# Kernel optimization log

Measured on AMD Instinct MI355X. Metric: run time of the kernel, lower is better.

Reference implementation:

```python
import jax, jax.numpy as jnp
import numpy as np

N, E, A, S = 100000, 1600000, 500000, 50000
F_IN, W, LAYERS = 64, 64, 3


def setup_inputs() -> dict:
    key = jax.random.key(0)
    ks = jax.random.split(key, 20)

    def glorot(k, shape):
        fan_in = shape[-2]
        return jax.random.normal(k, shape, dtype=jnp.float32) / jnp.sqrt(jnp.float32(fan_in))

    return {
        "x": jax.random.normal(ks[0], (N, F_IN), dtype=jnp.float32),
        "edge_src": jax.random.randint(ks[1], (E,), 0, N, dtype=jnp.int32),
        "edge_dst": jax.random.randint(ks[2], (E,), 0, N, dtype=jnp.int32),
        "gather_idx": jax.random.randint(ks[3], (A,), 0, N, dtype=jnp.int32),
        "seg_idx": jax.random.randint(ks[4], (A,), 0, S, dtype=jnp.int32),
        # GraphConv 0: lin_root (no bias) + lin_rel (bias)
        "w_root0": glorot(ks[5], (F_IN, W)),
        "w_rel0": glorot(ks[6], (F_IN, W)),
        "b0": jnp.zeros((W,), jnp.float32),
        # hidden GraphConv layers, stacked
        "w_root_h": glorot(ks[7], (LAYERS - 1, W, W)),
        "w_rel_h": glorot(ks[8], (LAYERS - 1, W, W)),
        "b_h": jnp.zeros((LAYERS - 1, W), jnp.float32),
        # MLP head
        "fc1_w": glorot(ks[9], (W, W)),
        "fc1_b": jnp.zeros((W,), jnp.float32),
        "fc2_w": glorot(ks[10], (W, 32)),
        "fc2_b": jnp.zeros((32,), jnp.float32),
        "fc3_w": glorot(ks[11], (32, 2)),
        "fc3_b": jnp.zeros((2,), jnp.float32),
        "num_sets": S,
    }


def _graph_conv(h, edge_src, edge_dst, w_root, w_rel, b):
    # PyG GraphConv (aggr='add'): out_i = W_root h_i + W_rel * sum_{j->i} h_j + b
    agg = jax.ops.segment_sum(h[edge_src], edge_dst, num_segments=h.shape[0])
    return h @ w_root + agg @ w_rel + b


def reference(x, edge_src, edge_dst, gather_idx, seg_idx,
              w_root0, w_rel0, b0, w_root_h, w_rel_h, b_h,
              fc1_w, fc1_b, fc2_w, fc2_b, fc3_w, fc3_b, num_sets):
    h = jax.nn.elu(_graph_conv(x, edge_src, edge_dst, w_root0, w_rel0, b0))
    for i in range(w_root_h.shape[0]):
        h = jax.nn.elu(_graph_conv(h, edge_src, edge_dst, w_root_h[i], w_rel_h[i], b_h[i]))
    # set pooling: gather node rows then scatter_add into sets
    pooled = jax.ops.segment_sum(h[gather_idx], seg_idx, num_segments=num_sets)  # [S, W]
    h = jax.nn.elu(pooled @ fc1_w + fc1_b)
    # dropout p=0.5 is identity at inference
    h = jax.nn.elu(h @ fc2_w + fc2_b)
    logits = h @ fc3_w + fc3_b
    return jax.nn.log_softmax(logits, axis=1)
```

## Files before the change

kernel.cpp:

```cpp
#include <hip/hip_runtime.h>


#define FEAT 64
#define SH 9
#define BSZ 512
#define CH 512
#define CAP 12288
#define SCHUNK 1024
#define IDXE 256
#define HPAD 8
#define LCHUNK 3200

typedef unsigned short u16;
typedef unsigned char u8;
typedef __attribute__((ext_vector_type(8))) short bf16x8;
typedef __attribute__((ext_vector_type(4))) float f32x4;
typedef __attribute__((ext_vector_type(2))) float f32x2;

__device__ __forceinline__ float bf2f(u16 u) {
  union { unsigned int i; float f; } c; c.i = ((unsigned int)u) << 16; return c.f;
}
__device__ __forceinline__ u16 f2bf(float f) {
  union { float f; unsigned int i; } c; c.f = f;
  unsigned int u = c.i;
  return (u16)((u + 0x7FFFu + ((u >> 16) & 1u)) >> 16);
}

__device__ __forceinline__ unsigned pack_fp8x4(float a, float b, float c, float d) {
  int lo = __builtin_amdgcn_cvt_pk_fp8_f32(a, b, 0, 0);
  return (unsigned)__builtin_amdgcn_cvt_pk_fp8_f32(c, d, lo, 1);
}
__device__ __forceinline__ float4 unpack_fp8x4(unsigned v) {
  f32x2 lo = __builtin_amdgcn_cvt_pk_f32_fp8(v, 0);
  f32x2 hi = __builtin_amdgcn_cvt_pk_f32_fp8(v, 1);
  float4 r; r.x = lo.x; r.y = lo.y; r.z = hi.x; r.w = hi.y;
  return r;
}

__global__ void p1a2f_kernel(const int* __restrict__ kE, int* __restrict__ cE, int nE, int NBe,
                             const int* __restrict__ kP, int* __restrict__ cP, int nP, int NBp,
                             const float* __restrict__ x, u16* __restrict__ xb,
                             u8* __restrict__ xb8, int n4, int g_cvt,
                             const float* __restrict__ wr0, const float* __restrict__ wl0,
                             const float* __restrict__ wrh, const float* __restrict__ wlh,
                             u16* __restrict__ wpack) {
  __shared__ int hist[256];
  int tid = threadIdx.x, b = blockIdx.x;
  if (b < 2 * CH) {
    const int* keys; int* counts; int nK, NB, c;
    if (b < CH) { keys = kE; counts = cE; nK = nE; NB = NBe; c = b; }
    else        { keys = kP; counts = cP; nK = nP; NB = NBp; c = b - CH; }
    hist[tid] = 0;
    __syncthreads();
    int len = (nK + CH - 1) / CH;
    int cbeg = c * len, cend = min(nK, cbeg + len);
    for (int i = cbeg + tid; i < cend; i += 256) atomicAdd(&hist[keys[i] >> SH], 1);
    __syncthreads();
    if (tid < NB) counts[tid * CH + c] = hist[tid];
  } else if (b < 2 * CH + g_cvt) {
    int i = (b - 2 * CH) * 256 + tid;
    if (i < n4) {
      float4 v = ((const float4*)x)[i];
      ushort4 o = { f2bf(v.x), f2bf(v.y), f2bf(v.z), f2bf(v.w) };
      ((ushort4*)xb)[i] = o;
      ((unsigned*)xb8)[i] = pack_fp8x4(v.x, v.y, v.z, v.w);
    }
  } else {
    int t4 = (b - 2 * CH - g_cvt) * 4 + (tid >> 6);
    if (t4 < 48) {
      int l = t4 >> 4, t = t4 & 15;
      int kt = t >> 2, nt = t & 3;
      int lane = tid & 63;
      const float* wr; const float* wl;
      if (l == 0) { wr = wr0; wl = wl0; }
      else        { wr = wrh + (l - 1) * FEAT * FEAT; wl = wlh + (l - 1) * FEAT * FEAT; }
      int n = nt * 16 + (lane & 15);
      int k0 = kt * 32 + (lane >> 4) * 8;
      u16* dst = wpack + (((size_t)l * 16 + t) * 64 + lane) * 8;
#pragma unroll
      for (int j = 0; j < 8; ++j) {
        int k = k0 + j;
        float v = (k < FEAT) ? wr[k * FEAT + n] : wl[(k - FEAT) * FEAT + n];
        dst[j] = f2bf(v);
      }
    } else if (t4 == 48) {
      int lane = tid & 63;
      int Nn = n4 >> 4;
      if (lane < 16) {
        ushort4 z = {0, 0, 0, 0};
        ((ushort4*)(xb + (size_t)Nn * FEAT))[lane] = z;
      } else if (lane < 32) {
        ((unsigned*)(xb8 + (size_t)Nn * FEAT))[lane & 15] = 0u;
      }
    }
  }
}

__global__ void scan1_kernel(int* __restrict__ d0, int* __restrict__ bs0, int L0, int nb0,
                             int* __restrict__ d1, int* __restrict__ bs1, int L1) {
  __shared__ int tsum[256];
  int tid = threadIdx.x, b = blockIdx.x;
  int* data; int* bsums; int L, c;
  if (b < nb0) { data = d0; bsums = bs0; L = L0; c = b; }
  else         { data = d1; bsums = bs1; L = L1; c = b - nb0; }
  int base = c * SCHUNK + tid * 4;
  int v[4];
#pragma unroll
  for (int i = 0; i < 4; ++i) v[i] = (base + i < L) ? data[base + i] : 0;
  int local = v[0] + v[1] + v[2] + v[3];
  tsum[tid] = local;
  __syncthreads();
  for (int off = 1; off < 256; off <<= 1) {
    int u = (tid >= off) ? tsum[tid - off] : 0;
    __syncthreads();
    tsum[tid] += u;
    __syncthreads();
  }
  int excl = tsum[tid] - local;
  if (tid == 255) bsums[c] = tsum[255];
  int run = excl;
#pragma unroll
  for (int i = 0; i < 4; ++i) {
    if (base + i < L) data[base + i] = run;
    run += v[i];
  }
}

__global__ void scan3_kernel(int* __restrict__ d0, const int* __restrict__ bs0,
                             int* __restrict__ bb0, int L0, int NB0, int tot0, int nb0, int g0,
                             int* __restrict__ d1, const int* __restrict__ bs1,
                             int* __restrict__ bb1, int L1, int NB1, int tot1, int nb1) {
  __shared__ int t[256];
  int b = blockIdx.x, tid = threadIdx.x;
  int* data; const int* bsums; int* bbase; int L, NB, tot, nb, i;
  if (b < g0) { data = d0; bsums = bs0; bbase = bb0; L = L0; NB = NB0; tot = tot0; nb = nb0; i = b * 256 + tid; }
  else        { data = d1; bsums = bs1; bbase = bb1; L = L1; NB = NB1; tot = tot1; nb = nb1; i = (b - g0) * 256 + tid; }
  int v = (tid < nb) ? bsums[tid] : 0;
  t[tid] = v;
  __syncthreads();
  for (int off = 1; off < 256; off <<= 1) {
    int u = (tid >= off) ? t[tid - off] : 0;
    __syncthreads();
    t[tid] += u;
    __syncthreads();
  }
  int incl = t[tid];
  __syncthreads();
  t[tid] = incl - v;
  __syncthreads();
  if (i < L) {
    int val = data[i] + t[i / SCHUNK];
    data[i] = val;
    if ((i & (CH - 1)) == 0) bbase[i / CH] = val;
  }
  if (i == 0) bbase[NB] = tot;
}

__global__ void __launch_bounds__(256)
p1b2_kernel(const int* __restrict__ s0, const int* __restrict__ k0,
            const int* __restrict__ c0, int* __restrict__ bin0, int n0, int NB0,
            const int* __restrict__ s1, const int* __restrict__ k1,
            const int* __restrict__ c1, int* __restrict__ bin1, int n1, int NB1) {
  __shared__ int s_bin[LCHUNK];
  __shared__ unsigned char s_bu[LCHUNK];
  __shared__ int lcur[256];
  __shared__ int gdiff[256];
  __shared__ int ts[256];
  int tid = threadIdx.x, b = blockIdx.x;
  const int* src; const int* keys; const int* counts; int* bin; int nE, NB, c;
  if (b < CH) { src = s0; keys = k0; counts = c0; bin = bin0; nE = n0; NB = NB0; c = b; }
  else        { src = s1; keys = k1; counts = c1; bin = bin1; nE = n1; NB = NB1; c = b - CH; }
  int len = (nE + CH - 1) / CH;
  int cbeg = c * len, cend = min(nE, cbeg + len);
  int L = cend - cbeg;

  int cur = 0, v = 0;
  if (tid < NB) {
    int f = tid * CH + c;
    cur = counts[f];
    int nxt = (f + 1 < NB * CH) ? counts[f + 1] : nE;
    v = nxt - cur;
  }
  ts[tid] = v;
  __syncthreads();
  for (int off = 1; off < 256; off <<= 1) {
    int u = (tid >= off) ? ts[tid - off] : 0;
    __syncthreads();
    ts[tid] += u;
    __syncthreads();
  }
  int excl = ts[tid] - v;
  lcur[tid] = excl;
  gdiff[tid] = cur - excl;
  __syncthreads();

  if (L <= LCHUNK) {
    for (int i = cbeg + tid; i < cend; i += 256) {
      int k = keys[i];
      int bu = k >> SH;
      int pos = atomicAdd(&lcur[bu], 1);
      s_bin[pos] = (src[i] << SH) | (k & (BSZ - 1));
      s_bu[pos] = (unsigned char)bu;
    }
    __syncthreads();
    for (int i = tid; i < L; i += 256) {
      int bu = s_bu[i];
      bin[gdiff[bu] + i] = s_bin[i];
    }
  } else {
    for (int i = cbeg + tid; i < cend; i += 256) {
      int k = keys[i];
      int bu = k >> SH;
      int pos = atomicAdd(&lcur[bu], 1);
      bin[gdiff[bu] + pos] = (src[i] << SH) | (k & (BSZ - 1));
    }
  }
}

__global__ void __launch_bounds__(256) p2_kernel(const int* __restrict__ bin0,
                                                 const int* __restrict__ bb0,
                                                 int* __restrict__ csr0, int* __restrict__ rs0,
                                                 int nn0, int NB0,
                                                 const int* __restrict__ bin1,
                                                 const int* __restrict__ bb1,
                                                 int* __restrict__ csr1, int* __restrict__ rs1,
                                                 int nn1) {
  __shared__ int s_csr[CAP];
  __shared__ int hist[BSZ];
  __shared__ int excl[BSZ];
  __shared__ int ts[256];
  int tid = threadIdx.x, bb = blockIdx.x;
  const int* bin; const int* bbase; int* csr; int* rs; int n_nodes, b;
  if (bb < NB0) { bin = bin0; bbase = bb0; csr = csr0; rs = rs0; n_nodes = nn0; b = bb; }
  else          { bin = bin1; bbase = bb1; csr = csr1; rs = rs1; n_nodes = nn1; b = bb - NB0; }
  int base = bbase[b];
  int cnt = bbase[b + 1] - base;
  int node_lo = b * BSZ;
  int nnode = min(BSZ, n_nodes - node_lo);

  hist[tid] = 0; hist[tid + 256] = 0;
  __syncthreads();
  for (int i = tid; i < cnt; i += 256) atomicAdd(&hist[bin[base + i] & (BSZ - 1)], 1);
  __syncthreads();

  int a0 = hist[2 * tid], a1 = hist[2 * tid + 1];
  int pair = a0 + a1;
  ts[tid] = pair;
  __syncthreads();
  for (int off = 1; off < 256; off <<= 1) {
    int u = (tid >= off) ? ts[tid - off] : 0;
    __syncthreads();
    ts[tid] += u;
    __syncthreads();
  }
  int pexcl = ts[tid] - pair;
  excl[2 * tid] = pexcl;
  excl[2 * tid + 1] = pexcl + a0;
  __syncthreads();

  for (int t = tid; t < nnode; t += 256) rs[node_lo + t] = base + excl[t];
  if (tid == 0 && node_lo + nnode >= n_nodes) rs[n_nodes] = bbase[(n_nodes + BSZ - 1) / BSZ];
  hist[tid] = excl[tid]; hist[tid + 256] = excl[tid + 256];
  __syncthreads();

  if (cnt <= CAP) {
    for (int i = tid; i < cnt; i += 256) {
      int e = bin[base + i];
      int pos = atomicAdd(&hist[e & (BSZ - 1)], 1);
      s_csr[pos] = e >> SH;
    }
    __syncthreads();
    for (int i = tid; i < cnt; i += 256) csr[base + i] = s_csr[i];
  } else {
    for (int i = tid; i < cnt; i += 256) {
      int e = bin[base + i];
      int pos = atomicAdd(&hist[e & (BSZ - 1)], 1);
      csr[base + pos] = e >> SH;
    }
  }
}

__device__ __forceinline__ float4 reduce_sub(float4 a) {
  a.x += __shfl_xor(a.x, 16, 64); a.y += __shfl_xor(a.y, 16, 64);
  a.z += __shfl_xor(a.z, 16, 64); a.w += __shfl_xor(a.w, 16, 64);
  a.x += __shfl_xor(a.x, 32, 64); a.y += __shfl_xor(a.y, 32, 64);
  a.z += __shfl_xor(a.z, 32, 64); a.w += __shfl_xor(a.w, 32, 64);
  return a;
}

struct RowB { ushort4 a, b, c, e; };

__device__ __forceinline__ RowB load_b16(const u16* __restrict__ hb, const int* idx,
                                         int i, int d, int ch, int sent) {
  int j0 = idx[i], j1 = idx[i + 4], j2 = idx[i + 8], j3 = idx[i + 12];
  j0 = (i      < d) ? j0 : sent;
  j1 = (i + 4  < d) ? j1 : sent;
  j2 = (i + 8  < d) ? j2 : sent;
  j3 = (i + 12 < d) ? j3 : sent;
  RowB r;
  r.a = ((const ushort4*)(hb + (size_t)((unsigned)(j0 * FEAT))))[ch];
  r.b = ((const ushort4*)(hb + (size_t)((unsigned)(j1 * FEAT))))[ch];
  r.c = ((const ushort4*)(hb + (size_t)((unsigned)(j2 * FEAT))))[ch];
  r.e = ((const ushort4*)(hb + (size_t)((unsigned)(j3 * FEAT))))[ch];
  return r;
}

__device__ __forceinline__ float4 acc_b16(float4 acc, RowB r) {
  acc.x += (bf2f(r.a.x) + bf2f(r.b.x)) + (bf2f(r.c.x) + bf2f(r.e.x));
  acc.y += (bf2f(r.a.y) + bf2f(r.b.y)) + (bf2f(r.c.y) + bf2f(r.e.y));
  acc.z += (bf2f(r.a.z) + bf2f(r.b.z)) + (bf2f(r.c.z) + bf2f(r.e.z));
  acc.w += (bf2f(r.a.w) + bf2f(r.b.w)) + (bf2f(r.c.w) + bf2f(r.e.w));
  return acc;
}

template <class FW>
__device__ __forceinline__ void gather8(const u16* __restrict__ hb,
                                        const int* __restrict__ rs,
                                        const int* __restrict__ csr,
                                        int* sidx, int wbase, int n, int sent,
                                        int sub, int ch, int lane, FW&& wr) {
  int r[9];
#pragma unroll
  for (int j = 0; j < 9; ++j) r[j] = rs[min(wbase + j, n)];
  int rbeg = r[0];
  int run = r[8] - rbeg;
  const int* eb;
  if (run <= IDXE) {
    for (int i = lane; i < run; i += 64) sidx[i] = csr[rbeg + i];
    eb = sidx;
  } else {
    eb = csr + rbeg;
  }
  int nt = min(8, n - wbase);
  if (nt == 8) {
    RowB fn = load_b16(hb, eb, sub, r[1] - r[0], ch, sent);
#pragma unroll
    for (int t = 0; t < 8; ++t) {
      int off = r[t] - rbeg;
      int d = r[t + 1] - r[t];
      RowB cur = fn;
      if (t < 7) fn = load_b16(hb, eb + (r[t + 1] - rbeg), sub, r[t + 2] - r[t + 1], ch, sent);
      float4 acc = {0.f, 0.f, 0.f, 0.f};
      for (int i = sub + 16; i < d; i += 16) {
        RowB nx = load_b16(hb, eb + off, i, d, ch, sent);
        acc = acc_b16(acc, cur);
        cur = nx;
      }
      acc = acc_b16(acc, cur);
      wr(t, reduce_sub(acc));
    }
  } else {
    for (int t = 0; t < nt; ++t) {
      int off = r[t] - rbeg;
      int d = r[t + 1] - r[t];
      float4 acc = {0.f, 0.f, 0.f, 0.f};
      for (int i = sub; i < d; i += 16)
        acc = acc_b16(acc, load_b16(hb, eb + off, i, d, ch, sent));
      wr(t, reduce_sub(acc));
    }
  }
}

struct Row8 { unsigned a, b, c, e; };

__device__ __forceinline__ Row8 load_b8(const u8* __restrict__ h8, const int* idx,
                                        int i, int d, int ch, int sent) {
  int j0 = idx[i], j1 = idx[i + 4], j2 = idx[i + 8], j3 = idx[i + 12];
  j0 = (i      < d) ? j0 : sent;
  j1 = (i + 4  < d) ? j1 : sent;
  j2 = (i + 8  < d) ? j2 : sent;
  j3 = (i + 12 < d) ? j3 : sent;
  Row8 r;
  r.a = ((const unsigned*)(h8 + (size_t)((unsigned)(j0 * FEAT))))[ch];
  r.b = ((const unsigned*)(h8 + (size_t)((unsigned)(j1 * FEAT))))[ch];
  r.c = ((const unsigned*)(h8 + (size_t)((unsigned)(j2 * FEAT))))[ch];
  r.e = ((const unsigned*)(h8 + (size_t)((unsigned)(j3 * FEAT))))[ch];
  return r;
}

__device__ __forceinline__ float4 acc_b8(float4 acc, Row8 r) {
  float4 A = unpack_fp8x4(r.a), B = unpack_fp8x4(r.b);
  float4 C = unpack_fp8x4(r.c), E = unpack_fp8x4(r.e);
  acc.x += (A.x + B.x) + (C.x + E.x);
  acc.y += (A.y + B.y) + (C.y + E.y);
  acc.z += (A.z + B.z) + (C.z + E.z);
  acc.w += (A.w + B.w) + (C.w + E.w);
  return acc;
}

template <class FW>
__device__ __forceinline__ void gather8q(const u8* __restrict__ h8,
                                         const int* __restrict__ rs,
                                         const int* __restrict__ csr,
                                         int* sidx, int wbase, int n, int sent,
                                         int sub, int ch, int lane, FW&& wr) {
  int r[9];
#pragma unroll
  for (int j = 0; j < 9; ++j) r[j] = rs[min(wbase + j, n)];
  int rbeg = r[0];
  int run = r[8] - rbeg;
  const int* eb;
  if (run <= IDXE) {
    for (int i = lane; i < run; i += 64) sidx[i] = csr[rbeg + i];
    eb = sidx;
  } else {
    eb = csr + rbeg;
  }
  int nt = min(8, n - wbase);
  if (nt == 8) {
    Row8 fn = load_b8(h8, eb, sub, r[1] - r[0], ch, sent);
#pragma unroll
    for (int t = 0; t < 8; ++t) {
      int off = r[t] - rbeg;
      int d = r[t + 1] - r[t];
      Row8 cur = fn;
      if (t < 7) fn = load_b8(h8, eb + (r[t + 1] - rbeg), sub, r[t + 2] - r[t + 1], ch, sent);
      float4 acc = {0.f, 0.f, 0.f, 0.f};
      for (int i = sub + 16; i < d; i += 16) {
        Row8 nx = load_b8(h8, eb + off, i, d, ch, sent);
        acc = acc_b8(acc, cur);
        cur = nx;
      }
      acc = acc_b8(acc, cur);
      wr(t, reduce_sub(acc));
    }
  } else {
    for (int t = 0; t < nt; ++t) {
      int off = r[t] - rbeg;
      int d = r[t + 1] - r[t];
      float4 acc = {0.f, 0.f, 0.f, 0.f};
      for (int i = sub; i < d; i += 16)
        acc = acc_b8(acc, load_b8(h8, eb + off, i, d, ch, sent));
      wr(t, reduce_sub(acc));
    }
  }
}

__global__ void __launch_bounds__(256, 8)
layer_fused_kernel(const u16* __restrict__ hb,
                   const u8* __restrict__ g8,
                   const int* __restrict__ rs,
                   const int* __restrict__ csr,
                   const u16* __restrict__ wpack,
                   const float* __restrict__ bias,
                   u16* __restrict__ outb,
                   u8* __restrict__ out8, int n) {
  __shared__ u16 s_h[32][FEAT + HPAD];
  __shared__ u16 s_a[32][FEAT + HPAD];
  __shared__ int s_idx[4][IDXE + 16];
  const int tid = threadIdx.x;
  const int wv = __builtin_amdgcn_readfirstlane(tid >> 6);
  const int lane = tid & 63;
  const int sub = lane >> 4;
  const int ch = lane & 15;
  const int base = blockIdx.x * 32;

  for (int it = 0; it < 2; ++it) {
    int idx = tid + it * 256;
    int nl = idx >> 4, c = idx & 15;
    int node = base + nl;
    if (node < n)
      *(ushort4*)&s_h[nl][c * 4] = ((const ushort4*)(hb + (size_t)node * FEAT))[c];
  }

  int wbase = base + wv * 8;
  if (wbase < n) {
    gather8q(g8, rs, csr, &s_idx[wv][0], wbase, n, n, sub, ch, lane,
             [&](int t, float4 acc) {
               if (sub == 0) {
                 ushort4 o = { f2bf(acc.x), f2bf(acc.y), f2bf(acc.z), f2bf(acc.w) };
                 *(ushort4*)&s_a[wv * 8 + t][ch * 4] = o;
               }
             });
  }
  __syncthreads();

  const int mt = wv & 1;
  const int ntb = (wv >> 1) * 2;
  const int mrow = mt * 16 + (lane & 15);
  const int koff = (lane >> 4) * 8;
  f32x4 acc0 = {0.f, 0.f, 0.f, 0.f};
  f32x4 acc1 = {0.f, 0.f, 0.f, 0.f};
#pragma unroll
  for (int kt = 0; kt < 4; ++kt) {
    bf16x8 a;
    if (kt < 2) a = *(const bf16x8*)&s_h[mrow][kt * 32 + koff];
    else        a = *(const bf16x8*)&s_a[mrow][(kt - 2) * 32 + koff];
    bf16x8 b0 = *(const bf16x8*)&wpack[(((size_t)kt * 4 + ntb) * 64 + lane) * 8];
    bf16x8 b1 = *(const bf16x8*)&wpack[(((size_t)kt * 4 + ntb + 1) * 64 + lane) * 8];
    acc0 = __builtin_amdgcn_mfma_f32_16x16x32_bf16(a, b0, acc0, 0, 0, 0);
    acc1 = __builtin_amdgcn_mfma_f32_16x16x32_bf16(a, b1, acc1, 0, 0, 0);
  }
  __syncthreads();

  const int col = lane & 15;
  const int rbase = (lane >> 4) * 4;
  const float bs0 = bias[ntb * 16 + col];
  const float bs1 = bias[(ntb + 1) * 16 + col];
#pragma unroll
  for (int rg = 0; rg < 4; ++rg) {
    int nl = mt * 16 + rbase + rg;
    float v0 = acc0[rg] + bs0;
    float v1 = acc1[rg] + bs1;
    v0 = v0 > 0.f ? v0 : (__expf(v0) - 1.f);
    v1 = v1 > 0.f ? v1 : (__expf(v1) - 1.f);
    s_h[nl][ntb * 16 + col] = f2bf(v0);
    s_h[nl][(ntb + 1) * 16 + col] = f2bf(v1);
  }
  __syncthreads();

  for (int it = 0; it < 2; ++it) {
    int idx = tid + it * 256;
    int nl = idx >> 4, c = idx & 15;
    int node = base + nl;
    if (node < n) {
      ushort4 v = *(const ushort4*)&s_h[nl][c * 4];
      ((ushort4*)(outb + (size_t)node * FEAT))[c] = v;
      if (out8)
        ((unsigned*)(out8 + (size_t)node * FEAT))[c] =
            pack_fp8x4(bf2f(v.x), bf2f(v.y), bf2f(v.z), bf2f(v.w));
    }
  }

  if (blockIdx.x == 0 && tid < 16) {
    ushort4 z = {0, 0, 0, 0};
    ((ushort4*)(outb + (size_t)n * FEAT))[tid] = z;
    if (out8) ((unsigned*)(out8 + (size_t)n * FEAT))[tid] = 0u;
  }
}

__global__ void __launch_bounds__(512)
pool_mlp_kernel(const u16* __restrict__ hb,
                const int* __restrict__ rs,
                const int* __restrict__ csr,
                const float* __restrict__ fc1_w, const float* __restrict__ fc1_b,
                const float* __restrict__ fc2_w, const float* __restrict__ fc2_b,
                const float* __restrict__ fc3_w, const float* __restrict__ fc3_b,
                float* __restrict__ out, int nsets, int nnodes) {
  __shared__ float s_p[64][FEAT + 4];
  __shared__ int s_idx[8][IDXE + 16];
  const int tid = threadIdx.x;
  const int wv = __builtin_amdgcn_readfirstlane(tid >> 6);
  const int lane = tid & 63;
  const int sub = lane >> 4;
  const int ch = lane & 15;
  const int base = blockIdx.x * 64;

  int wbase = base + wv * 8;
  if (wbase < nsets) {
    gather8(hb, rs, csr, &s_idx[wv][0], wbase, nsets, nnodes, sub, ch, lane,
            [&](int t, float4 acc) {
              if (sub == 0) *(float4*)&s_p[wv * 8 + t][ch * 4] = acc;
            });
  }
  __syncthreads();

  {
    const int jb = wv * 8;
    float acc[8];
#pragma unroll
    for (int jj = 0; jj < 8; ++jj) acc[jj] = fc1_b[jb + jj];
    for (int k = 0; k < FEAT; k += 4) {
      const float4 pv = *(const float4*)&s_p[lane][k];
      const float pk[4] = {pv.x, pv.y, pv.z, pv.w};
#pragma unroll
      for (int kk = 0; kk < 4; ++kk) {
        const float* w = fc1_w + (k + kk) * FEAT + jb;
#pragma unroll
        for (int jj = 0; jj < 8; ++jj) acc[jj] += pk[kk] * w[jj];
      }
    }
    __syncthreads();
#pragma unroll
    for (int jj = 0; jj < 8; ++jj) {
      float a = acc[jj];
      s_p[lane][jb + jj] = a > 0.f ? a : (__expf(a) - 1.f);
    }
  }
  __syncthreads();

  {
    const int jb = wv * 4;
    float acc[4];
#pragma unroll
    for (int jj = 0; jj < 4; ++jj) acc[jj] = fc2_b[jb + jj];
    for (int k = 0; k < FEAT; k += 4) {
      const float4 tv = *(const float4*)&s_p[lane][k];
      const float tk[4] = {tv.x, tv.y, tv.z, tv.w};
#pragma unroll
      for (int kk = 0; kk < 4; ++kk) {
        const float* w = fc2_w + (k + kk) * 32 + jb;
#pragma unroll
        for (int jj = 0; jj < 4; ++jj) acc[jj] += tk[kk] * w[jj];
      }
    }
    __syncthreads();
#pragma unroll
    for (int jj = 0; jj < 4; ++jj) {
      float a = acc[jj];
      s_p[lane][jb + jj] = a > 0.f ? a : (__expf(a) - 1.f);
    }
  }
  __syncthreads();

  if (wv == 0) {
    int s = base + lane;
    if (s < nsets) {
      float a0 = fc3_b[0], a1 = fc3_b[1];
      for (int k = 0; k < 32; k += 4) {
        const float4 tv = *(const float4*)&s_p[lane][k];
        const float tk[4] = {tv.x, tv.y, tv.z, tv.w};
#pragma unroll
        for (int kk = 0; kk < 4; ++kk) {
          a0 += tk[kk] * fc3_w[(k + kk) * 2 + 0];
          a1 += tk[kk] * fc3_w[(k + kk) * 2 + 1];
        }
      }
      float m = fmaxf(a0, a1);
      float lse = m + logf(__expf(a0 - m) + __expf(a1 - m));
      float2 r = {a0 - lse, a1 - lse};
      *(float2*)(out + (size_t)s * 2) = r;
    }
  }
}

extern "C" void kernel_launch(void* const* d_in, const int* in_sizes, int n_in,
                              void* d_out, int out_size, void* d_ws, size_t ws_size,
                              hipStream_t stream) {
  const float* x        = (const float*)d_in[0];
  const int* edge_src   = (const int*)d_in[1];
  const int* edge_dst   = (const int*)d_in[2];
  const int* gather_idx = (const int*)d_in[3];
  const int* seg_idx    = (const int*)d_in[4];
  const float* w_root0  = (const float*)d_in[5];
  const float* w_rel0   = (const float*)d_in[6];
  const float* b0       = (const float*)d_in[7];
  const float* w_root_h = (const float*)d_in[8];
  const float* w_rel_h  = (const float*)d_in[9];
  const float* b_h      = (const float*)d_in[10];
  const float* fc1_w    = (const float*)d_in[11];
  const float* fc1_b    = (const float*)d_in[12];
  const float* fc2_w    = (const float*)d_in[13];
  const float* fc2_b    = (const float*)d_in[14];
  const float* fc3_w    = (const float*)d_in[15];
  const float* fc3_b    = (const float*)d_in[16];

  const int N = in_sizes[0] / FEAT;
  const int E = in_sizes[1];
  const int A = in_sizes[3];
  const int S = out_size / 2;

  const int NB_e = (N + BSZ - 1) / BSZ;
  const int NB_p = (S + BSZ - 1) / BSZ;
  const int L_e = NB_e * CH, L_p = NB_p * CH;
  const int nb_e = (L_e + SCHUNK - 1) / SCHUNK;
  const int nb_p = (L_p + SCHUNK - 1) / SCHUNK;
  const int g_e = (L_e + 255) / 256, g_p = (L_p + 255) / 256;

  size_t hrow_bytes = (size_t)(N + 1) * FEAT * sizeof(u16);
  size_t h8_bytes   = (size_t)(N + 1) * FEAT;
  char* ws = (char*)d_ws;
  size_t off = 0;
  auto alloc = [&](size_t bytes) { void* p = ws + off; off += (bytes + 15) & ~(size_t)15; return p; };
  u16* xb       = (u16*)alloc(hrow_bytes);
  u16* b1b      = (u16*)alloc(hrow_bytes);
  u16* b2b      = (u16*)alloc(hrow_bytes);
  u8* xb8       = (u8*)alloc(h8_bytes);
  u8* h8a       = (u8*)alloc(h8_bytes);
  u8* h8b       = (u8*)alloc(h8_bytes);
  int* csr_e    = (int*)alloc((size_t)(E + 16) * 4);
  int* bin_e    = (int*)alloc((size_t)E * 4);
  int* rs_e     = (int*)alloc((size_t)(N + 1) * 4);
  int* counts_e = (int*)alloc((size_t)L_e * 4);
  int* bbase_e  = (int*)alloc((size_t)(NB_e + 1) * 4);
  int* csr_p    = (int*)alloc((size_t)(A + 16) * 4);
  int* bin_p    = (int*)alloc((size_t)A * 4);
  int* rs_p     = (int*)alloc((size_t)(S + 1) * 4);
  int* counts_p = (int*)alloc((size_t)L_p * 4);
  int* bbase_p  = (int*)alloc((size_t)(NB_p + 1) * 4);
  int* bsums_e  = (int*)alloc(256 * 4);
  int* bsums_p  = (int*)alloc(256 * 4);
  u16* wpack    = (u16*)alloc((size_t)3 * 16 * 64 * 8 * sizeof(u16));

  dim3 blk(256);
  dim3 blk512(512);

  int n4 = N * FEAT / 4;
  int g_cvt = (n4 + 255) / 256;
  int g_pp = 13;

  p1a2f_kernel<<<2 * CH + g_cvt + g_pp, blk, 0, stream>>>(
      edge_dst, counts_e, E, NB_e, seg_idx, counts_p, A, NB_p,
      x, xb, xb8, n4, g_cvt, w_root0, w_rel0, w_root_h, w_rel_h, wpack);
  scan1_kernel<<<nb_e + nb_p, blk, 0, stream>>>(counts_e, bsums_e, L_e, nb_e,
                                                counts_p, bsums_p, L_p);
  scan3_kernel<<<g_e + g_p, blk, 0, stream>>>(counts_e, bsums_e, bbase_e, L_e, NB_e, E, nb_e, g_e,
                                              counts_p, bsums_p, bbase_p, L_p, NB_p, A, nb_p);
  p1b2_kernel<<<2 * CH, blk, 0, stream>>>(edge_src, edge_dst, counts_e, bin_e, E, NB_e,
                                          gather_idx, seg_idx, counts_p, bin_p, A, NB_p);
  p2_kernel<<<NB_e + NB_p, blk, 0, stream>>>(bin_e, bbase_e, csr_e, rs_e, N, NB_e,
                                             bin_p, bbase_p, csr_p, rs_p, S);

  int lgrid = (N + 31) / 32;
  int pgrid = (S + 63) / 64;

  layer_fused_kernel<<<lgrid, blk, 0, stream>>>(xb, xb8, rs_e, csr_e, wpack,
                                                b0, b1b, h8a, N);
  layer_fused_kernel<<<lgrid, blk, 0, stream>>>(b1b, h8a, rs_e, csr_e, wpack + 16 * 64 * 8,
                                                b_h, b2b, h8b, N);
  layer_fused_kernel<<<lgrid, blk, 0, stream>>>(b2b, h8b, rs_e, csr_e, wpack + 2 * 16 * 64 * 8,
                                                b_h + FEAT, b1b, (u8*)nullptr, N);

  pool_mlp_kernel<<<pgrid, blk512, 0, stream>>>(b1b, rs_p, csr_p,
                                                fc1_w, fc1_b, fc2_w, fc2_b, fc3_w, fc3_b,
                                                (float*)d_out, S, N);
}
```

Baseline: 271.2 us.

## Fuse scan and bin-scatter kernels into one cooperative kernel with grid syncs

Result: slower. 524.6 us (+93.4%).

```diff
diff --git a/kernel.cpp b/kernel.cpp
--- a/kernel.cpp
+++ b/kernel.cpp
@@ -1,4 +1,7 @@
 #include <hip/hip_runtime.h>
+#include <hip/hip_cooperative_groups.h>
+
+namespace cg = cooperative_groups;
 
 
 #define FEAT 64
@@ -26,7 +29,11 @@
   return (u16)((u + 0x7FFFu + ((u >> 16) & 1u)) >> 16);
 }
 
+__device__ __forceinline__ float clamp448(float v) {
+  return fminf(fmaxf(v, -448.f), 448.f);
+}
 __device__ __forceinline__ unsigned pack_fp8x4(float a, float b, float c, float d) {
+  a = clamp448(a); b = clamp448(b); c = clamp448(c); d = clamp448(d);
   int lo = __builtin_amdgcn_cvt_pk_fp8_f32(a, b, 0, 0);
   return (unsigned)__builtin_amdgcn_cvt_pk_fp8_f32(c, d, lo, 1);
 }
@@ -213,6 +220,128 @@
       int bu = k >> SH;
       int pos = atomicAdd(&lcur[bu], 1);
       bin[gdiff[bu] + pos] = (src[i] << SH) | (k & (BSZ - 1));
+    }
+  }
+}
+
+__global__ void __launch_bounds__(256)
+build2_kernel(int* counts_e, int* bsums_e, int L_e, int nb_e,
+              int* counts_p, int* bsums_p, int L_p, int nb_p,
+              int* bbase_e, int NB_e, int totE, int g_e3, int g_p3,
+              int* bbase_p, int NB_p, int totA,
+              const int* s0, const int* k0, int* bin0,
+              const int* s1, const int* k1, int* bin1) {
+  __shared__ int s_bin[LCHUNK];
+  __shared__ unsigned char s_bu[LCHUNK];
+  __shared__ int lcur[256];
+  __shared__ int gdiff[256];
+  __shared__ int ts[256];
+  cg::grid_group grid = cg::this_grid();
+  int tid = threadIdx.x, b = blockIdx.x;
+
+  if (b < nb_e + nb_p) {
+    int* data; int* bsums; int L, c;
+    if (b < nb_e) { data = counts_e; bsums = bsums_e; L = L_e; c = b; }
+    else          { data = counts_p; bsums = bsums_p; L = L_p; c = b - nb_e; }
+    int base = c * SCHUNK + tid * 4;
+    int v[4];
+#pragma unroll
+    for (int i = 0; i < 4; ++i) v[i] = (base + i < L) ? data[base + i] : 0;
+    int local = v[0] + v[1] + v[2] + v[3];
+    ts[tid] = local;
+    __syncthreads();
+    for (int off = 1; off < 256; off <<= 1) {
+      int u = (tid >= off) ? ts[tid - off] : 0;
+      __syncthreads();
+      ts[tid] += u;
+      __syncthreads();
+    }
+    int excl = ts[tid] - local;
+    if (tid == 255) bsums[c] = ts[255];
+    int run = excl;
+#pragma unroll
+    for (int i = 0; i < 4; ++i) {
+      if (base + i < L) data[base + i] = run;
+      run += v[i];
+    }
+  }
+  grid.sync();
+
+  if (b < g_e3 + g_p3) {
+    int* data; const int* bsums; int* bbase; int L, NB, tot, nb, i;
+    if (b < g_e3) { data = counts_e; bsums = bsums_e; bbase = bbase_e; L = L_e; NB = NB_e; tot = totE; nb = nb_e; i = b * 256 + tid; }
+    else          { data = counts_p; bsums = bsums_p; bbase = bbase_p; L = L_p; NB = NB_p; tot = totA; nb = nb_p; i = (b - g_e3) * 256 + tid; }
+    int v = (tid < nb) ? bsums[tid] : 0;
+    ts[tid] = v;
+    __syncthreads();
+    for (int off = 1; off < 256; off <<= 1) {
+      int u = (tid >= off) ? ts[tid - off] : 0;
+      __syncthreads();
+      ts[tid] += u;
+      __syncthreads();
+    }
+    int incl = ts[tid];
+    __syncthreads();
+    ts[tid] = incl - v;
+    __syncthreads();
+    if (i < L) {
+      int val = data[i] + ts[i / SCHUNK];
+      data[i] = val;
+      if ((i & (CH - 1)) == 0) bbase[i / CH] = val;
+    }
+    if (i == 0) bbase[NB] = tot;
+  }
+  grid.sync();
+
+  {
+    const int* src; const int* keys; const int* counts; int* bin; int nE, NB, c;
+    if (b < CH) { src = s0; keys = k0; counts = counts_e; bin = bin0; nE = totE; NB = NB_e; c = b; }
+    else        { src = s1; keys = k1; counts = counts_p; bin = bin1; nE = totA; NB = NB_p; c = b - CH; }
+    int len = (nE + CH - 1) / CH;
+    int cbeg = c * len, cend = min(nE, cbeg + len);
+    int L = cend - cbeg;
+
+    int cur = 0, v = 0;
+    if (tid < NB) {
+      int f = tid * CH + c;
+      cur = counts[f];
+      int nxt = (f + 1 < NB * CH) ? counts[f + 1] : nE;
+      v = nxt - cur;
+    }
+    __syncthreads();
+    ts[tid] = v;
+    __syncthreads();
+    for (int off = 1; off < 256; off <<= 1) {
+      int u = (tid >= off) ? ts[tid - off] : 0;
+      __syncthreads();
+      ts[tid] += u;
+      __syncthreads();
+    }
+    int excl = ts[tid] - v;
+    lcur[tid] = excl;
+    gdiff[tid] = cur - excl;
+    __syncthreads();
+
+    if (L <= LCHUNK) {
+      for (int i = cbeg + tid; i < cend; i += 256) {
+        int k = keys[i];
+        int bu = k >> SH;
+        int pos = atomicAdd(&lcur[bu], 1);
+        s_bin[pos] = (src[i] << SH) | (k & (BSZ - 1));
+        s_bu[pos] = (unsigned char)bu;
+      }
+      __syncthreads();
+      for (int i = tid; i < L; i += 256) {
+        int bu = s_bu[i];
+        bin[gdiff[bu] + i] = s_bin[i];
+      }
+    } else {
+      for (int i = cbeg + tid; i < cend; i += 256) {
+        int k = keys[i];
+        int bu = k >> SH;
+        int pos = atomicAdd(&lcur[bu], 1);
+        bin[gdiff[bu] + pos] = (src[i] << SH) | (k & (BSZ - 1));
+      }
     }
   }
 }
@@ -692,12 +821,42 @@
   p1a2f_kernel<<<2 * CH + g_cvt + g_pp, blk, 0, stream>>>(
       edge_dst, counts_e, E, NB_e, seg_idx, counts_p, A, NB_p,
       x, xb, xb8, n4, g_cvt, w_root0, w_rel0, w_root_h, w_rel_h, wpack);
-  scan1_kernel<<<nb_e + nb_p, blk, 0, stream>>>(counts_e, bsums_e, L_e, nb_e,
-                                                counts_p, bsums_p, L_p);
-  scan3_kernel<<<g_e + g_p, blk, 0, stream>>>(counts_e, bsums_e, bbase_e, L_e, NB_e, E, nb_e, g_e,
-                                              counts_p, bsums_p, bbase_p, L_p, NB_p, A, nb_p);
-  p1b2_kernel<<<2 * CH, blk, 0, stream>>>(edge_src, edge_dst, counts_e, bin_e, E, NB_e,
-                                          gather_idx, seg_idx, counts_p, bin_p, A, NB_p);
+
+  static int build2_ok = -1;
+  if (build2_ok < 0) {
+    int per = 0, cus = 0;
+    hipError_t e1 = hipOccupancyMaxActiveBlocksPerMultiprocessor(
+        &per, (const void*)build2_kernel, 256, 0);
+    hipError_t e2 = hipDeviceGetAttribute(&cus, hipDeviceAttributeMultiprocessorCount, 0);
+    build2_ok = (e1 == hipSuccess && e2 == hipSuccess && per * cus >= 2 * CH) ? 1 : 0;
+  }
+  bool did_coop = false;
+  if (build2_ok) {
+    int vL_e = L_e, vnb_e = nb_e, vL_p = L_p, vnb_p = nb_p;
+    int vNB_e = NB_e, vE = E, vg_e = g_e, vg_p = g_p, vNB_p = NB_p, vA = A;
+    const int* vsrc0 = edge_src; const int* vkey0 = edge_dst;
+    const int* vsrc1 = gather_idx; const int* vkey1 = seg_idx;
+    void* args[] = {
+      (void*)&counts_e, (void*)&bsums_e, (void*)&vL_e, (void*)&vnb_e,
+      (void*)&counts_p, (void*)&bsums_p, (void*)&vL_p, (void*)&vnb_p,
+      (void*)&bbase_e, (void*)&vNB_e, (void*)&vE, (void*)&vg_e, (void*)&vg_p,
+      (void*)&bbase_p, (void*)&vNB_p, (void*)&vA,
+      (void*)&vsrc0, (void*)&vkey0, (void*)&bin_e,
+      (void*)&vsrc1, (void*)&vkey1, (void*)&bin_p
+    };
+    hipError_t err = hipLaunchCooperativeKernel(build2_kernel, dim3(2 * CH), dim3(256),
+                                                args, 0, stream);
+    did_coop = (err == hipSuccess);
+  }
+  if (!did_coop) {
+    scan1_kernel<<<nb_e + nb_p, blk, 0, stream>>>(counts_e, bsums_e, L_e, nb_e,
+                                                  counts_p, bsums_p, L_p);
+    scan3_kernel<<<g_e + g_p, blk, 0, stream>>>(counts_e, bsums_e, bbase_e, L_e, NB_e, E, nb_e, g_e,
+                                                counts_p, bsums_p, bbase_p, L_p, NB_p, A, nb_p);
+    p1b2_kernel<<<2 * CH, blk, 0, stream>>>(edge_src, edge_dst, counts_e, bin_e, E, NB_e,
+                                            gather_idx, seg_idx, counts_p, bin_p, A, NB_p);
+  }
+
   p2_kernel<<<NB_e + NB_p, blk, 0, stream>>>(bin_e, bbase_e, csr_e, rs_e, N, NB_e,
                                              bin_p, bbase_p, csr_p, rs_p, S);
 
```
